# Performance work log

Measured on AMD Instinct MI355X. Metric: run time of the kernel, lower is better.

## Reference

```python
import jax, jax.numpy as jnp
import numpy as np

N_TOKENS = 8192
D_MODEL = 1024
HD_DIM = 4096
N_VEC = 32
N_EXP = 12


def setup_inputs() -> dict:
    key = jax.random.key(0)
    k1, k2, k3, k4, k5 = jax.random.split(key, 5)
    # Glorot-style scaling for the bases so activations stay O(1)
    s_up = (2.0 / (D_MODEL + HD_DIM)) ** 0.5
    return {
        "inputs": jax.random.normal(k1, (N_TOKENS, D_MODEL), dtype=jnp.float32),
        "shared_basis_up": jax.random.normal(k2, (N_VEC, D_MODEL, HD_DIM), dtype=jnp.float32) * s_up,
        "shared_basis_down": jax.random.normal(k3, (N_VEC, HD_DIM, D_MODEL), dtype=jnp.float32) * s_up,
        "expert_coeffs_up": jax.random.normal(k4, (N_EXP, N_VEC), dtype=jnp.float32) * 0.5,
        "expert_coeffs_down": jax.random.normal(k5, (N_EXP, N_VEC), dtype=jnp.float32) * 0.5,
        "expert_bias": jnp.zeros((N_EXP, D_MODEL), dtype=jnp.float32),
        "expert_idx": 3,
    }


def reference(inputs, shared_basis_up, shared_basis_down, expert_coeffs_up,
              expert_coeffs_down, expert_bias, expert_idx):
    coeffs_up = expert_coeffs_up[expert_idx]      # [v]
    coeffs_down = expert_coeffs_down[expert_idx]  # [v]
    bias = expert_bias[expert_idx]                # [d_model]
    # Reconstruct expert weights from shared basis
    W_up = jnp.einsum('v,vdh->dh', coeffs_up, shared_basis_up)      # [d_model, hd_dim]
    W_down = jnp.einsum('v,vhd->hd', coeffs_down, shared_basis_down)  # [hd_dim, d_model]
    hidden = jax.nn.gelu(inputs @ W_up, approximate=False)  # TF default gelu is exact (erf)
    return hidden @ W_down + bias
```

## Files before the change

### kernel.cpp

```cpp
#include <hip/hip_runtime.h>
#include <cstdint>

#define NTOK 8192
#define DMODEL 1024
#define HDDIM 4096
#define NVEC 32

typedef float f32x4_v __attribute__((ext_vector_type(4)));
typedef __bf16 bf16x8 __attribute__((ext_vector_type(8)));
typedef unsigned short u16x4 __attribute__((ext_vector_type(4)));
typedef unsigned short u16x8 __attribute__((ext_vector_type(8)));

__device__ __forceinline__ unsigned short f2bf(float f) {
  union { float f; uint32_t u; } x; x.f = f;
  uint32_t r = (x.u + 0x7FFFu + ((x.u >> 16) & 1u)) >> 16;
  return (unsigned short)r;
}

__device__ __forceinline__ float gelu_fast(float x) {
  float t = x * x;
  float z = x * (2.3022082f + 0.1029440f * t);
  float e = exp2f(-z);
  return x / (1.0f + e);
}

#define VMCNT(n) asm volatile("s_waitcnt vmcnt(" #n ")" ::: "memory")

__device__ __forceinline__ void gload16(const unsigned short* g, unsigned short* lds)
{
  __builtin_amdgcn_global_load_lds((__attribute__((address_space(1))) void*)g,
                                   (__attribute__((address_space(3))) void*)lds,
                                   16, 0, 0);
}

__device__ __forceinline__
void reconstruct_body(const float* __restrict__ basis,
                      const float* __restrict__ coeffs,
                      int e, unsigned short* __restrict__ outT,
                      int X, int Y, int tile, int bid, char* smem)
{
  float (*lds)[260] = (float (*)[260])smem;
  const int xtiles = X >> 4;
  const int bx = tile % xtiles;
  const int by = tile / xtiles;
  const int x0 = bx << 4, y0 = by << 8;
  const int t  = threadIdx.x;
  const int w  = t >> 6, l = t & 63;

  f32x4_v acc[4];
  #pragma unroll
  for (int i = 0; i < 4; ++i) acc[i] = (f32x4_v){0.f, 0.f, 0.f, 0.f};

  const size_t mat = (size_t)X * (size_t)Y;
  uint32_t roff[4];
  #pragma unroll
  for (int i = 0; i < 4; ++i)
    roff[i] = (uint32_t)(x0 + w * 4 + i) * (uint32_t)Y + (uint32_t)(y0 + l * 4);

  #pragma unroll 4
  for (int vv = 0; vv < NVEC; ++vv) {
    const int v = (vv + bid) & (NVEC - 1);
    const float cv = coeffs[e * NVEC + v];
    const float* pv = basis + (size_t)v * mat;
    #pragma unroll
    for (int i = 0; i < 4; ++i) {
      f32x4_v d = __builtin_nontemporal_load((const f32x4_v*)(pv + roff[i]));
      acc[i] += cv * d;
    }
  }

  #pragma unroll
  for (int i = 0; i < 4; ++i)
    *(f32x4_v*)&lds[w * 4 + i][l * 4] = acc[i];
  __syncthreads();

  const int y = y0 + t;
  u16x8 o0, o1;
  #pragma unroll
  for (int x = 0; x < 8; ++x)  o0[x] = f2bf(lds[x][t]);
  #pragma unroll
  for (int x = 0; x < 8; ++x)  o1[x] = f2bf(lds[8 + x][t]);
  unsigned short* dst = outT + (size_t)y * X + x0;
  *(u16x8*)dst = o0;
  *(u16x8*)(dst + 8) = o1;
}

#define CVT_BLKS 512

__global__ __launch_bounds__(256)
void mem_kernel(const float* __restrict__ inputs,
                const float* __restrict__ basis_up,
                const float* __restrict__ basis_down,
                const float* __restrict__ cup,
                const float* __restrict__ cdn,
                const int* __restrict__ eidx_p,
                unsigned short* __restrict__ A_bf,
                unsigned short* __restrict__ WupT,
                unsigned short* __restrict__ WdnT)
{
  __shared__ __align__(16) char smem[16 * 260 * 4];
  const int bid = blockIdx.x;
  if (bid < 1024) {
    reconstruct_body(basis_up, cup, *eidx_p, WupT, DMODEL, HDDIM, bid, bid, smem);
  } else if (bid < 2048) {
    reconstruct_body(basis_down, cdn, *eidx_p, WdnT, HDDIM, DMODEL, bid - 1024, bid, smem);
  } else {
    const int n4 = NTOK * DMODEL / 4;
    const int stride = CVT_BLKS * 256;
    for (int i = (bid - 2048) * 256 + threadIdx.x; i < n4; i += stride) {
      f32x4_v v = ((const f32x4_v*)inputs)[i];
      u16x4 u;
      #pragma unroll
      for (int j = 0; j < 4; ++j) u[j] = f2bf(v[j]);
      ((u16x4*)A_bf)[i] = u;
    }
  }
}

template<int BM, int BN, int CHM, int CHN>
__global__ __launch_bounds__(512)
void gemm8p(const unsigned short* __restrict__ A,
            const unsigned short* __restrict__ Bt,
            unsigned short* __restrict__ Cbf,
            int M, int N, int K)
{
  constexpr int BK   = 32;
  constexpr int FM   = BM / 32;
  constexpr int FN   = BN / 64;
  constexpr int P    = (FM * FN) / 16;
  constexpr int SLOT = (BM + BN) * BK * 2;
  constexpr int L    = SLOT / 16 / 512;
  constexpr int LPP  = L / P;
  constexpr int ACH  = BM * 4;
  constexpr int JA   = ACH / 512;

  __shared__ __align__(16) char smem[4 * SLOT];

  const int nb  = N / BN;
  const int ncn = nb / CHN;
  const int xcd = blockIdx.x & 7;
  const int idx = blockIdx.x >> 3;
  const int bm  = (xcd / ncn) * CHM + idx / CHN;
  const int bn  = (xcd % ncn) * CHN + idx % CHN;
  const int m0 = bm * BM, n0 = bn * BN;

  const int tid = threadIdx.x;
  const int w = tid >> 6, l = tid & 63;
  const int wm = w >> 2, wn = w & 3;
  const int lrow = l & 15, lkc = l >> 4;

  uint32_t soff[L];
  #pragma unroll
  for (int j = 0; j < L; ++j) {
    const int q = tid + j * 512;
    if (j < JA) {
      const int r = q >> 2, cs = (q & 3) ^ ((r >> 1) & 3);
      soff[j] = (uint32_t)(m0 + r) * (uint32_t)K + cs * 8;
    } else {
      const int q2 = q - ACH;
      const int r = q2 >> 2, cs = (q2 & 3) ^ ((r >> 1) & 3);
      soff[j] = (uint32_t)(n0 + r) * (uint32_t)K + cs * 8;
    }
  }

  int aoff[FM], boff[FN];
  #pragma unroll
  for (int f = 0; f < FM; ++f) {
    const int r = wm * (BM / 2) + f * 16 + lrow;
    aoff[f] = r * 64 + ((lkc ^ ((r >> 1) & 3)) << 4);
  }
  #pragma unroll
  for (int n_ = 0; n_ < FN; ++n_) {
    const int r = wn * (BN / 4) + n_ * 16 + lrow;
    boff[n_] = BM * 64 + r * 64 + ((lkc ^ ((r >> 1) & 3)) << 4);
  }

  f32x4_v acc[FM][FN];
  #pragma unroll
  for (int f = 0; f < FM; ++f)
    #pragma unroll
    for (int n_ = 0; n_ < FN; ++n_) acc[f][n_] = (f32x4_v){0.f, 0.f, 0.f, 0.f};

  const int NT = K / BK;

  for (int tt = 0; tt < 3; ++tt) {
    char* sb = smem + tt * SLOT;
    #pragma unroll
    for (int j = 0; j < L; ++j)
      gload16((j < JA ? A : Bt) + soff[j] + tt * BK,
              (unsigned short*)(sb + (tid + j * 512) * 16));
  }
  VMCNT(8);
  __builtin_amdgcn_s_barrier();
  __builtin_amdgcn_sched_barrier(0);

  bf16x8 bfr[FN];
  for (int t = 0; t < NT; ++t) {
    const char* sb = smem + (t & 3) * SLOT;
    char* pb = smem + ((t + 3) & 3) * SLOT;
    const bool do_stage = (t + 3 < NT);
    #pragma unroll
    for (int p = 0; p < P; ++p) {
      bf16x8 af[4];
      #pragma unroll
      for (int m_ = 0; m_ < 4; ++m_)
        af[m_] = *(const bf16x8*)(sb + aoff[p * 4 + m_]);
      if (p == 0) {
        #pragma unroll
        for (int n_ = 0; n_ < FN; ++n_)
          bfr[n_] = *(const bf16x8*)(sb + boff[n_]);
      }
      if (do_stage) {
        #pragma unroll
        for (int jj = 0; jj < LPP; ++jj) {
          const int j = p * LPP + jj;
          gload16((j < JA ? A : Bt) + soff[j] + (t + 3) * BK,
                  (unsigned short*)(pb + (tid + j * 512) * 16));
        }
      }
      __builtin_amdgcn_s_barrier();
      __builtin_amdgcn_s_setprio(1);
      #pragma unroll
      for (int m_ = 0; m_ < 4; ++m_)
        #pragma unroll
        for (int n_ = 0; n_ < FN; ++n_)
          acc[p * 4 + m_][n_] = __builtin_amdgcn_mfma_f32_16x16x32_bf16(
              af[m_], bfr[n_], acc[p * 4 + m_][n_], 0, 0, 0);
      __builtin_amdgcn_s_setprio(0);
      if (p == P - 1) {
        if (t < NT - 3)       { VMCNT(8); }
        else if (t == NT - 3) { VMCNT(4); }
        else if (t == NT - 2) { VMCNT(0); }
      }
      __builtin_amdgcn_s_barrier();
      __builtin_amdgcn_sched_barrier(0);
    }
  }

  const int colq = l & 15;
  const int rowq = (l >> 4) * 4;
  #pragma unroll
  for (int f = 0; f < FM; ++f)
    #pragma unroll
    for (int n_ = 0; n_ < FN; ++n_) {
      const int col = n0 + wn * (BN / 4) + n_ * 16 + colq;
      #pragma unroll
      for (int r = 0; r < 4; ++r) {
        const int row = m0 + wm * (BM / 2) + f * 16 + rowq + r;
        Cbf[(size_t)row * N + col] = f2bf(gelu_fast(acc[f][n_][r]));
      }
    }
}

template<int CHM, int CHN>
__global__ __launch_bounds__(512)
void gemm_k64(const unsigned short* __restrict__ A,
              const unsigned short* __restrict__ Bt,
              float* __restrict__ Cf,
              const float* __restrict__ bias,
              const int* __restrict__ eidx_p,
              int M, int N, int K)
{
  constexpr int BM = 128, BN = 256, BK = 64;
  constexpr int SLOT = (BM + BN) * BK * 2;
  constexpr int L = 6, JA = 2;
  __shared__ __align__(16) char smem[3 * SLOT];

  const int nb  = N / BN;
  const int ncn = nb / CHN;
  const int xcd = blockIdx.x & 7;
  const int idx = blockIdx.x >> 3;
  const int bm  = (xcd / ncn) * CHM + idx / CHN;
  const int bn  = (xcd % ncn) * CHN + idx % CHN;
  const int m0 = bm * BM, n0 = bn * BN;

  const int tid = threadIdx.x;
  const int w = tid >> 6, l = tid & 63;
  const int wm = w >> 2, wn = w & 3;
  const int lrow = l & 15, lkc = l >> 4;

  uint32_t soff[L];
  #pragma unroll
  for (int j = 0; j < L; ++j) {
    const int q = tid + j * 512;
    if (j < JA) {
      const int r = q >> 3, cs = (q & 7) ^ (r & 7);
      soff[j] = (uint32_t)(m0 + r) * (uint32_t)K + cs * 8;
    } else {
      const int q2 = q - 1024;
      const int r = q2 >> 3, cs = (q2 & 7) ^ (r & 7);
      soff[j] = (uint32_t)(n0 + r) * (uint32_t)K + cs * 8;
    }
  }

  int abase[4], aswz[4], bbase[4], bswz[4];
  #pragma unroll
  for (int f = 0; f < 4; ++f) {
    const int r = wm * 64 + f * 16 + lrow;
    abase[f] = r * 128; aswz[f] = r & 7;
  }
  #pragma unroll
  for (int n_ = 0; n_ < 4; ++n_) {
    const int r = wn * 64 + n_ * 16 + lrow;
    bbase[n_] = 16384 + r * 128; bswz[n_] = r & 7;
  }

  f32x4_v acc[4][4];
  #pragma unroll
  for (int f = 0; f < 4; ++f)
    #pragma unroll
    for (int n_ = 0; n_ < 4; ++n_) acc[f][n_] = (f32x4_v){0.f, 0.f, 0.f, 0.f};

  const int NT = K / BK;

  for (int tt = 0; tt < 2; ++tt) {
    char* sb = smem + tt * SLOT;
    #pragma unroll
    for (int j = 0; j < L; ++j)
      gload16((j < JA ? A : Bt) + soff[j] + tt * BK,
              (unsigned short*)(sb + (tid + j * 512) * 16));
  }
  VMCNT(6);
  __builtin_amdgcn_s_barrier();
  __builtin_amdgcn_sched_barrier(0);

  int cur = 0, pf = 2;
  for (int t = 0; t < NT; ++t) {
    const char* sb = smem + cur * SLOT;
    char* pb = smem + pf * SLOT;
    const bool do_stage = (t + 2 < NT);
    #pragma unroll
    for (int p = 0; p < 2; ++p) {
      bf16x8 af[4], bfr[4];
      #pragma unroll
      for (int m_ = 0; m_ < 4; ++m_)
        af[m_] = *(const bf16x8*)(sb + abase[m_] + ((((p << 2) + lkc) ^ aswz[m_]) << 4));
      #pragma unroll
      for (int n_ = 0; n_ < 4; ++n_)
        bfr[n_] = *(const bf16x8*)(sb + bbase[n_] + ((((p << 2) + lkc) ^ bswz[n_]) << 4));
      if (do_stage) {
        #pragma unroll
        for (int jj = 0; jj < 3; ++jj) {
          const int j = p * 3 + jj;
          gload16((j < JA ? A : Bt) + soff[j] + (t + 2) * BK,
                  (unsigned short*)(pb + (tid + j * 512) * 16));
        }
      }
      __builtin_amdgcn_s_barrier();
      __builtin_amdgcn_s_setprio(1);
      #pragma unroll
      for (int m_ = 0; m_ < 4; ++m_)
        #pragma unroll
        for (int n_ = 0; n_ < 4; ++n_)
          acc[m_][n_] = __builtin_amdgcn_mfma_f32_16x16x32_bf16(
              af[m_], bfr[n_], acc[m_][n_], 0, 0, 0);
      __builtin_amdgcn_s_setprio(0);
      if (p == 1) {
        if (t < NT - 2)       { VMCNT(6); }
        else if (t == NT - 2) { VMCNT(0); }
      }
      __builtin_amdgcn_s_barrier();
      __builtin_amdgcn_sched_barrier(0);
    }
    cur = (cur == 2) ? 0 : cur + 1;
    pf  = (pf == 2) ? 0 : pf + 1;
  }

  const int colq = l & 15;
  const int rowq = (l >> 4) * 4;
  const int e = *eidx_p;
  const float* brow = bias + (size_t)e * N;
  #pragma unroll
  for (int n_ = 0; n_ < 4; ++n_) {
    const int col = n0 + wn * 64 + n_ * 16 + colq;
    const float bv = brow[col];
    #pragma unroll
    for (int f = 0; f < 4; ++f)
      #pragma unroll
      for (int r = 0; r < 4; ++r) {
        const int row = m0 + wm * 64 + f * 16 + rowq + r;
        Cf[(size_t)row * N + col] = acc[f][n_][r] + bv;
      }
  }
}

extern "C" void kernel_launch(void* const* d_in, const int* in_sizes, int n_in,
                              void* d_out, int out_size, void* d_ws, size_t ws_size,
                              hipStream_t stream)
{
  const float* inputs     = (const float*)d_in[0];
  const float* basis_up   = (const float*)d_in[1];
  const float* basis_down = (const float*)d_in[2];
  const float* cup        = (const float*)d_in[3];
  const float* cdn        = (const float*)d_in[4];
  const float* bias       = (const float*)d_in[5];
  const int*   eidx       = (const int*)d_in[6];
  float*       out        = (float*)d_out;

  char* ws = (char*)d_ws;
  unsigned short* A_bf   = (unsigned short*)(ws);
  unsigned short* hidden = (unsigned short*)(ws + (16u << 20));
  unsigned short* WupT   = (unsigned short*)(ws + (80u << 20));
  unsigned short* WdnT   = (unsigned short*)(ws + (88u << 20));

  mem_kernel<<<2560, 256, 0, stream>>>(
      inputs, basis_up, basis_down, cup, cdn, eidx, A_bf, WupT, WdnT);

  gemm8p<256, 256, 8, 8><<<512, 512, 0, stream>>>(
      A_bf, WupT, hidden, NTOK, HDDIM, DMODEL);

  gemm_k64<8, 4><<<256, 512, 0, stream>>>(
      hidden, WdnT, out, bias, eidx, NTOK, DMODEL, HDDIM);
}
```

Baseline: 353.4 us.

## Overlap W_down reconstruction with first GEMM by interleaving blocks

Moves the down-projection weight reconstruction out of the first memory kernel and into the first GEMM launch. Odd blocks reconstruct two W_down tiles, each with half the threads, while even blocks run GEMM tiles. The aim is to hide the memory-bound basis_down reads (512MB fp32) behind the compute-bound GEMM. The risks are that the GEMM-tile-to-XCD mapping changes because tiles are now indexed by bid>>1, and that reconstruct blocks sit in 512-thread blocks with large LDS, which may lower occupancy.

```diff
diff --git a/kernel.cpp b/kernel.cpp
--- a/kernel.cpp
+++ b/kernel.cpp
@@ -37,14 +37,13 @@
 void reconstruct_body(const float* __restrict__ basis,
                       const float* __restrict__ coeffs,
                       int e, unsigned short* __restrict__ outT,
-                      int X, int Y, int tile, int bid, char* smem)
+                      int X, int Y, int tile, int stag, char* smem, int t)
 {
   float (*lds)[260] = (float (*)[260])smem;
   const int xtiles = X >> 4;
   const int bx = tile % xtiles;
   const int by = tile / xtiles;
   const int x0 = bx << 4, y0 = by << 8;
-  const int t  = threadIdx.x;
   const int w  = t >> 6, l = t & 63;
 
   f32x4_v acc[4];
@@ -59,7 +58,7 @@
 
   #pragma unroll 4
   for (int vv = 0; vv < NVEC; ++vv) {
-    const int v = (vv + bid) & (NVEC - 1);
+    const int v = (vv + stag) & (NVEC - 1);
     const float cv = coeffs[e * NVEC + v];
     const float* pv = basis + (size_t)v * mat;
     #pragma unroll
@@ -85,29 +84,23 @@
   *(u16x8*)(dst + 8) = o1;
 }
 
-#define CVT_BLKS 512
-
 __global__ __launch_bounds__(256)
-void mem_kernel(const float* __restrict__ inputs,
-                const float* __restrict__ basis_up,
-                const float* __restrict__ basis_down,
-                const float* __restrict__ cup,
-                const float* __restrict__ cdn,
-                const int* __restrict__ eidx_p,
-                unsigned short* __restrict__ A_bf,
-                unsigned short* __restrict__ WupT,
-                unsigned short* __restrict__ WdnT)
+void p1_kernel(const float* __restrict__ inputs,
+               const float* __restrict__ basis_up,
+               const float* __restrict__ cup,
+               const int* __restrict__ eidx_p,
+               unsigned short* __restrict__ A_bf,
+               unsigned short* __restrict__ WupT)
 {
   __shared__ __align__(16) char smem[16 * 260 * 4];
   const int bid = blockIdx.x;
   if (bid < 1024) {
-    reconstruct_body(basis_up, cup, *eidx_p, WupT, DMODEL, HDDIM, bid, bid, smem);
-  } else if (bid < 2048) {
-    reconstruct_body(basis_down, cdn, *eidx_p, WdnT, HDDIM, DMODEL, bid - 1024, bid, smem);
+    reconstruct_body(basis_up, cup, *eidx_p, WupT, DMODEL, HDDIM, bid, bid,
+                     smem, threadIdx.x);
   } else {
     const int n4 = NTOK * DMODEL / 4;
-    const int stride = CVT_BLKS * 256;
-    for (int i = (bid - 2048) * 256 + threadIdx.x; i < n4; i += stride) {
+    const int stride = 512 * 256;
+    for (int i = (bid - 1024) * 256 + threadIdx.x; i < n4; i += stride) {
       f32x4_v v = ((const f32x4_v*)inputs)[i];
       u16x4 u;
       #pragma unroll
@@ -117,29 +110,41 @@
   }
 }
 
-template<int BM, int BN, int CHM, int CHN>
 __global__ __launch_bounds__(512)
-void gemm8p(const unsigned short* __restrict__ A,
-            const unsigned short* __restrict__ Bt,
-            unsigned short* __restrict__ Cbf,
-            int M, int N, int K)
-{
-  constexpr int BK   = 32;
-  constexpr int FM   = BM / 32;
-  constexpr int FN   = BN / 64;
-  constexpr int P    = (FM * FN) / 16;
+void p2_kernel(const unsigned short* __restrict__ A,
+               const unsigned short* __restrict__ Bt,
+               unsigned short* __restrict__ Cbf,
+               const float* __restrict__ basis_down,
+               const float* __restrict__ cdn,
+               const int* __restrict__ eidx_p,
+               unsigned short* __restrict__ WdnT)
+{
+  constexpr int BM = 256, BN = 256, BK = 32, CHM = 8, CHN = 8;
+  constexpr int FM = BM / 32, FN = BN / 64;
+  constexpr int P = (FM * FN) / 16;
   constexpr int SLOT = (BM + BN) * BK * 2;
-  constexpr int L    = SLOT / 16 / 512;
-  constexpr int LPP  = L / P;
-  constexpr int ACH  = BM * 4;
-  constexpr int JA   = ACH / 512;
+  constexpr int L = SLOT / 16 / 512;
+  constexpr int LPP = L / P;
+  constexpr int ACH = BM * 4;
+  constexpr int JA = ACH / 512;
 
   __shared__ __align__(16) char smem[4 * SLOT];
 
-  const int nb  = N / BN;
-  const int ncn = nb / CHN;
-  const int xcd = blockIdx.x & 7;
-  const int idx = blockIdx.x >> 3;
+  const int bid = blockIdx.x;
+
+  if (bid & 1) {
+    const int half = threadIdx.x >> 8;
+    const int tile = (bid >> 1) * 2 + half;
+    reconstruct_body(basis_down, cdn, *eidx_p, WdnT, HDDIM, DMODEL,
+                     tile, bid + half, smem + half * 16640, threadIdx.x & 255);
+    return;
+  }
+
+  const int gtile = bid >> 1;
+  const int K = DMODEL, N = HDDIM;
+  const int ncn = (N / BN) / CHN;
+  const int xcd = gtile & 7;
+  const int idx = gtile >> 3;
   const int bm  = (xcd / ncn) * CHM + idx / CHN;
   const int bn  = (xcd % ncn) * CHN + idx % CHN;
   const int m0 = bm * BM, n0 = bn * BN;
@@ -403,11 +408,11 @@
   unsigned short* WupT   = (unsigned short*)(ws + (80u << 20));
   unsigned short* WdnT   = (unsigned short*)(ws + (88u << 20));
 
-  mem_kernel<<<2560, 256, 0, stream>>>(
-      inputs, basis_up, basis_down, cup, cdn, eidx, A_bf, WupT, WdnT);
-
-  gemm8p<256, 256, 8, 8><<<512, 512, 0, stream>>>(
-      A_bf, WupT, hidden, NTOK, HDDIM, DMODEL);
+  p1_kernel<<<1536, 256, 0, stream>>>(
+      inputs, basis_up, cup, eidx, A_bf, WupT);
+
+  p2_kernel<<<1024, 512, 0, stream>>>(
+      A_bf, WupT, hidden, basis_down, cdn, eidx, WdnT);
 
   gemm_k64<8, 4><<<256, 512, 0, stream>>>(
       hidden, WdnT, out, bias, eidx, NTOK, DMODEL, HDDIM);
```

After: 318.2 us (median of 2 runs). 10.0% less time.
